# Kernel optimization log

Measured on AMD Instinct MI355X. Metric: run time of the kernel, lower is better.

Reference implementation:

```python
import jax, jax.numpy as jnp
import numpy as np

N = 4096
FIN = 512
HID = 256
NCLS = 2
NE = 131072

def _glorot(key, fan_in, fan_out):
    r = np.sqrt(6.0 / (fan_in + fan_out))
    return jax.random.uniform(key, (fan_in, fan_out), jnp.float32, -r, r)

def setup_inputs() -> dict:
    key = jax.random.key(0)
    ks = jax.random.split(key, 16)
    X = jax.random.normal(ks[0], (N, FIN), jnp.float32)
    adj_rows = jax.random.randint(ks[1], (NE,), 0, N, jnp.int32)
    adj_cols = jax.random.randint(ks[2], (NE,), 0, N, jnp.int32)
    adj_vals = jax.random.uniform(ks[3], (NE,), jnp.float32)
    W_shared = _glorot(ks[4], FIN, HID)
    W_iv = _glorot(ks[5], HID, HID)
    W_c = _glorot(ks[6], HID, HID)
    W_r = _glorot(ks[7], HID, HID)
    Wg_iv = _glorot(ks[8], HID, HID)
    Wg_c = _glorot(ks[9], HID, HID)
    Wg_r = _glorot(ks[10], HID, HID)
    lin_W = _glorot(ks[11], 2 * HID, NCLS)
    lin_b = jnp.zeros((NCLS,), jnp.float32)
    return {"X": X, "adj_rows": adj_rows, "adj_cols": adj_cols, "adj_vals": adj_vals,
            "W_shared": W_shared, "W_iv": W_iv, "W_c": W_c, "W_r": W_r,
            "Wg_iv": Wg_iv, "Wg_c": Wg_c, "Wg_r": Wg_r, "lin_W": lin_W, "lin_b": lin_b}

def _spmm(rows, cols, vals, m):
    # sparse.mm(adj, m): out[i] = sum_{e: rows[e]==i} vals[e] * m[cols[e]]
    return jax.ops.segment_sum(vals[:, None] * m[cols], rows, num_segments=N)

def _gcn(x, rows, cols, vals, W):
    # dropout is identity in eval mode
    return jax.nn.relu(_spmm(rows, cols, vals, x @ W))

def _graphite(x, r1, r2, W):
    h = x @ W
    return jax.nn.relu(r1 @ (r1.T @ h) + r2 @ (r2.T @ h))

def reference(X, adj_rows, adj_cols, adj_vals, W_shared, W_iv, W_c, W_r, Wg_iv, Wg_c, Wg_r, lin_W, lin_b):
    h = _gcn(X, adj_rows, adj_cols, adj_vals, W_shared)
    z_iv0 = _gcn(h, adj_rows, adj_cols, adj_vals, W_iv)
    z_c0 = _gcn(h, adj_rows, adj_cols, adj_vals, W_c)
    z_r0 = _gcn(h, adj_rows, adj_cols, adj_vals, W_r)
    z_iv_rec0 = z_iv0 @ z_iv0.T
    z_c_rec0 = z_c0 @ z_c0.T
    z_r_rec0 = z_r0 @ z_r0.T
    A_dense = jnp.zeros((N, N), jnp.float32).at[adj_rows, adj_cols].add(adj_vals)
    z_iv = _graphite(z_iv0, A_dense, jax.nn.sigmoid(z_iv_rec0), Wg_iv)
    z_c = _graphite(z_c0, A_dense, jax.nn.sigmoid(z_c_rec0), Wg_c)
    z_r = _graphite(z_r0, A_dense, jax.nn.sigmoid(z_r_rec0), Wg_r)
    z_iv_rec = z_iv @ z_iv.T
    z_c_rec = z_c @ z_c.T
    z_r_rec = z_r @ z_r.T
    concat = jnp.concatenate([z_iv, z_c], axis=1)
    pred_T = jax.nn.log_softmax(concat @ lin_W + lin_b, axis=1)
    mi_total_loss = jnp.array(0.0, jnp.float32)
    return (z_iv, z_iv_rec, z_c, z_c_rec, z_r, z_r_rec, mi_total_loss, pred_T)
```

## Files before the change

### kernel.cpp

```cpp
#include <hip/hip_runtime.h>

#define Nn   4096
#define FINd 512
#define HIDd 256
#define NEd  131072

typedef unsigned short u16;
typedef __bf16 bf16x8 __attribute__((ext_vector_type(8)));
typedef float floatx4 __attribute__((ext_vector_type(4)));

__device__ __forceinline__ float bf2f(u16 u) {
  union { unsigned int i; float f; } v; v.i = ((unsigned int)u) << 16; return v.f;
}
__device__ __forceinline__ u16 f2bf(float f) {
  union { unsigned int i; float f; } v; v.f = f;
  unsigned int x = v.i;
  return (u16)((x + 0x7FFFu + ((x >> 16) & 1u)) >> 16);
}

#define GLDS(gp, lp) __builtin_amdgcn_global_load_lds( \
    (__attribute__((address_space(1))) unsigned int*)(void*)(gp), \
    (__attribute__((address_space(3))) unsigned int*)(lp), 16, 0, 0)

__global__ __launch_bounds__(256) void hist_priv_k(const int* __restrict__ rows,
                                                   const int* __restrict__ cols,
                                                   int* __restrict__ slabs) {
  __shared__ int cnt[8192];
  const int t = threadIdx.x;
  for (int i = t; i < 8192; i += 256) cnt[i] = 0;
  __syncthreads();
  int base = blockIdx.x * 4096;
  for (int i = t; i < 4096; i += 256) {
    int e = base + i;
    atomicAdd(&cnt[rows[e]], 1);
    atomicAdd(&cnt[4096 + cols[e]], 1);
  }
  __syncthreads();
  int* out = slabs + blockIdx.x * 8192;
  for (int i = t; i < 8192; i += 256) out[i] = cnt[i];
}

__global__ __launch_bounds__(1024) void scan2_k(const unsigned int* __restrict__ X,
                                                const int* __restrict__ slabs,
                                                int* __restrict__ rp, int* __restrict__ cp,
                                                int* __restrict__ rfill, int* __restrict__ cfill,
                                                int* __restrict__ flag) {
  __shared__ int part[1024];
  __shared__ int dcnt;
  const int t = threadIdx.x;
  if (t == 0) dcnt = 0;
  __syncthreads();
  int local = 0;
  for (int i = t; i < 4096; i += 1024) {
    unsigned e = (X[i] >> 7) & 0xFFu;
    if (e >= 100u && e <= 140u) local++;
  }
  if (local) atomicAdd(&dcnt, local);
  int base = t * 8, s = 0, loc[8];
  int csum[8];
#pragma unroll
  for (int j = 0; j < 8; ++j) csum[j] = 0;
  for (int sl = 0; sl < 32; ++sl) {
    const int* sp = slabs + sl * 8192 + base;
#pragma unroll
    for (int j = 0; j < 8; ++j) csum[j] += sp[j];
  }
#pragma unroll
  for (int j = 0; j < 8; ++j) { loc[j] = s; s += csum[j]; }
  part[t] = s;
  __syncthreads();
  if (t == 0) *flag = (dcnt > 2458) ? 1 : 0;
  for (int off = 1; off < 1024; off <<= 1) {
    int v = (t >= off) ? part[t - off] : 0;
    __syncthreads();
    part[t] += v;
    __syncthreads();
  }
  int excl = (t == 0) ? 0 : part[t - 1];
  int rtot = part[511];
  if (t < 512) {
#pragma unroll
    for (int j = 0; j < 8; ++j) rp[base + j] = excl + loc[j];
    if (t == 511) rp[4096] = rtot;
  } else {
    int cb = base - 4096;
    int ex2 = excl - rtot;
#pragma unroll
    for (int j = 0; j < 8; ++j) cp[cb + j] = ex2 + loc[j];
    if (t == 1023) cp[4096] = part[1023] - rtot;
  }
  for (int i = t; i < 4096; i += 1024) { rfill[i] = 0; cfill[i] = 0; }
}

__global__ __launch_bounds__(256) void setup2_k(const void* __restrict__ X,
                                                const void* __restrict__ Wsh,
                                                const void* __restrict__ W0, const void* __restrict__ W1,
                                                const void* __restrict__ W2, const void* __restrict__ G0,
                                                const void* __restrict__ G1, const void* __restrict__ G2,
                                                const void* __restrict__ linW, const void* __restrict__ linb,
                                                const int* __restrict__ rows, const int* __restrict__ cols,
                                                const void* __restrict__ vals,
                                                const int* __restrict__ rp, const int* __restrict__ cp,
                                                int* __restrict__ rfill, int* __restrict__ cfill,
                                                int2* __restrict__ rpack, int2* __restrict__ cpack,
                                                u16* __restrict__ Xb, u16* __restrict__ WshT,
                                                u16* __restrict__ WTb, u16* __restrict__ WgTb,
                                                float* __restrict__ linWf, float* __restrict__ linbf,
                                                const int* __restrict__ flag) {
  int fl = *flag;
  int bx = blockIdx.x;
  if (bx >= 10245) {
    int e = (bx - 10245) * 256 + threadIdx.x;
    if (e >= NEd) return;
    float v = fl ? bf2f(((const u16*)vals)[e]) : ((const float*)vals)[e];
    int r = rows[e], c = cols[e];
    int p1 = rp[r] + atomicAdd(&rfill[r], 1);
    rpack[p1] = make_int2(c, __float_as_int(v));
    int p2 = cp[c] + atomicAdd(&cfill[c], 1);
    cpack[p2] = make_int2(r, __float_as_int(v));
    return;
  }
  int i = bx * 256 + threadIdx.x;
  if (i < 2097152) {
    Xb[i] = fl ? ((const u16*)X)[i] : f2bf(((const float*)X)[i]);
    return;
  }
  int i2 = i - 2097152;
  if (i2 < 131072) {
    int r = i2 >> 8, c = i2 & 255;
    u16 v = fl ? ((const u16*)Wsh)[i2] : f2bf(((const float*)Wsh)[i2]);
    WshT[c * 512 + r] = v;
    return;
  }
  int i3 = i2 - 131072;
  if (i3 < 393216) {
    int w = i3 >> 16, j = i3 & 65535;
    int r = j >> 8, c = j & 255;
    const void* src = (w == 0) ? W0 : (w == 1) ? W1 : (w == 2) ? W2
                     : (w == 3) ? G0 : (w == 4) ? G1 : G2;
    u16 v = fl ? ((const u16*)src)[j] : f2bf(((const float*)src)[j]);
    u16* dst = (w < 3) ? (WTb + w * 65536) : (WgTb + (w - 3) * 65536);
    dst[c * 256 + r] = v;
    return;
  }
  int i4 = i3 - 393216;
  if (i4 < 1024) { linWf[i4] = fl ? bf2f(((const u16*)linW)[i4]) : ((const float*)linW)[i4]; return; }
  if (i4 < 1026) { int k = i4 - 1024; linbf[k] = fl ? bf2f(((const u16*)linb)[k]) : ((const float*)linb)[k]; }
}

struct SPP {
  const int* ptr; const int2* ep;
  const u16* m[3]; u16* ob[3]; unsigned long long oo[3];
};
__global__ __launch_bounds__(256) void spmm_mb_k(SPP s, const float* __restrict__ part,
                                                 void* __restrict__ outbase, int mode,
                                                 const int* __restrict__ flag) {
  const int b = blockIdx.y;
  int gid = blockIdx.x * 256 + threadIdx.x;
  int row = gid >> 6, lane = gid & 63, f = lane << 2;
  int beg = s.ptr[row], end = s.ptr[row + 1];
  const u16* m = s.m[b];
  float ax = 0.f, ay = 0.f, az = 0.f, aw = 0.f;
  for (int e = beg; e < end; ++e) {
    int2 cv = s.ep[e];
    float v = __int_as_float(cv.y);
    ushort4 mv = *(const ushort4*)(m + (size_t)cv.x * HIDd + f);
    ax = fmaf(v, bf2f(mv.x), ax);
    ay = fmaf(v, bf2f(mv.y), ay);
    az = fmaf(v, bf2f(mv.z), az);
    aw = fmaf(v, bf2f(mv.w), aw);
  }
  size_t o = (size_t)row * HIDd + f;
  if (mode == 2) {
    const float* pb = part + (size_t)b * 1048576 + o;
    float4 p0 = *(const float4*)(pb);
    float4 p1 = *(const float4*)(pb + 3145728);
    float4 p2 = *(const float4*)(pb + 2 * 3145728);
    float4 p3 = *(const float4*)(pb + 3 * 3145728);
    ax += p0.x + p1.x + p2.x + p3.x;
    ay += p0.y + p1.y + p2.y + p3.y;
    az += p0.z + p1.z + p2.z + p3.z;
    aw += p0.w + p1.w + p2.w + p3.w;
    ax = fmaxf(ax, 0.f); ay = fmaxf(ay, 0.f);
    az = fmaxf(az, 0.f); aw = fmaxf(aw, 0.f);
    ushort4 o4 = { f2bf(ax), f2bf(ay), f2bf(az), f2bf(aw) };
    *(ushort4*)(s.ob[b] + o) = o4;
    if (*flag) *(ushort4*)((u16*)outbase + s.oo[b] + o) = o4;
    else       *(float4*)((float*)outbase + s.oo[b] + o) = make_float4(ax, ay, az, aw);
  } else {
    if (mode == 0) {
      ax = fmaxf(ax, 0.f); ay = fmaxf(ay, 0.f);
      az = fmaxf(az, 0.f); aw = fmaxf(aw, 0.f);
    }
    ushort4 o4 = { f2bf(ax), f2bf(ay), f2bf(az), f2bf(aw) };
    *(ushort4*)(s.ob[b] + o) = o4;
  }
}

struct RSU {
  const float* part; u16* tT;
  const int* cp; const int2* cep;
  const u16* hp[3]; u16* ub[3];
};
__global__ __launch_bounds__(256) void redt_spmmu_k(RSU r) {
  int bx = blockIdx.x;
  if (bx < 3072) {
    int i = (bx * 256 + threadIdx.x) * 4;
    float4 s0 = *(const float4*)(r.part + i);
    float4 s1 = *(const float4*)(r.part + i + 3145728);
    float4 s2 = *(const float4*)(r.part + i + 2 * 3145728);
    float4 s3 = *(const float4*)(r.part + i + 3 * 3145728);
    ushort4 o = { f2bf(s0.x + s1.x + s2.x + s3.x), f2bf(s0.y + s1.y + s2.y + s3.y),
                  f2bf(s0.z + s1.z + s2.z + s3.z), f2bf(s0.w + s1.w + s2.w + s3.w) };
    *(ushort4*)(r.tT + i) = o;
    return;
  }
  int bb = (bx - 3072) >> 10;
  int gid = ((bx - 3072) & 1023) * 256 + threadIdx.x;
  int row = gid >> 6, lane = gid & 63, f = lane << 2;
  int beg = r.cp[row], end = r.cp[row + 1];
  const u16* m = r.hp[bb];
  float ax = 0.f, ay = 0.f, az = 0.f, aw = 0.f;
  for (int e = beg; e < end; ++e) {
    int2 cv = r.cep[e];
    float v = __int_as_float(cv.y);
    ushort4 mv = *(const ushort4*)(m + (size_t)cv.x * HIDd + f);
    ax = fmaf(v, bf2f(mv.x), ax);
    ay = fmaf(v, bf2f(mv.y), ay);
    az = fmaf(v, bf2f(mv.z), az);
    aw = fmaf(v, bf2f(mv.w), aw);
  }
  size_t o = (size_t)row * HIDd + f;
  ushort4 o4 = { f2bf(ax), f2bf(ay), f2bf(az), f2bf(aw) };
  *(ushort4*)(r.ub[bb] + o) = o4;
}

struct Job {
  const u16* A; const u16* B;
  const float* F1; const float* F2;
  unsigned long long c0, c1, pstride;
  int M, N, K, mode, xt, ntiles, nks, kspan, sym;
};
struct Jobs { Job j[6]; };

__global__ __launch_bounds__(256) void gemm_mega(Jobs P, void* __restrict__ WSv,
                                                 void* __restrict__ OutO,
                                                 const int* __restrict__ flag) {
  __shared__ __align__(16) u16 smem[17408];
  u16* As = smem;
  u16* Bs = smem + 8192;
  u16* Ts = smem;
  const Job jb = P.j[blockIdx.z];
  const unsigned tile = blockIdx.x;
  if ((int)tile >= jb.ntiles * jb.nks) return;
  if (jb.mode == 6) {
    int i = tile * 256 + threadIdx.x;
    const float* lw = jb.F1;
    float a0 = jb.F2[0], a1 = jb.F2[1];
    for (int f = 0; f < HIDd; ++f) {
      float zv = bf2f(jb.A[(size_t)i * HIDd + f]);
      a0 = fmaf(zv, lw[2 * f + 0], a0);
      a1 = fmaf(zv, lw[2 * f + 1], a1);
    }
    for (int f = 0; f < HIDd; ++f) {
      float zv = bf2f(jb.B[(size_t)i * HIDd + f]);
      a0 = fmaf(zv, lw[2 * (HIDd + f) + 0], a0);
      a1 = fmaf(zv, lw[2 * (HIDd + f) + 1], a1);
    }
    float mx = fmaxf(a0, a1);
    float lse = mx + logf(expf(a0 - mx) + expf(a1 - mx));
    float p0 = a0 - lse, p1 = a1 - lse;
    if (*flag) {
      u16* ob = (u16*)OutO;
      ob[jb.c0 + 2 * i + 0] = f2bf(p0);
      ob[jb.c0 + 2 * i + 1] = f2bf(p1);
      if (i == 0) ob[jb.c1] = 0;
    } else {
      float* ob = (float*)OutO;
      ob[jb.c0 + 2 * i + 0] = p0;
      ob[jb.c0 + 2 * i + 1] = p1;
      if (i == 0) ob[jb.c1] = 0.f;
    }
    return;
  }
  const unsigned ks = tile / (unsigned)jb.ntiles;
  const unsigned t2 = tile - ks * jb.ntiles;
  unsigned ty, tx;
  if (jb.sym) {
    unsigned rem = t2, rowlen = jb.xt; ty = 0;
    while (rem >= rowlen) { rem -= rowlen; --rowlen; ++ty; }
    tx = ty + rem;
  } else {
    ty = t2 / (unsigned)jb.xt;
    tx = t2 - ty * jb.xt;
  }
  const int K = jb.K, N = jb.N;
  const int row0 = ty * 128, col0 = tx * 128;
  const int tid = threadIdx.x;
  const int w = tid >> 6, lane = tid & 63;
  const int wr = (w >> 1) * 64, wc = (w & 1) * 64;
  const int lr = lane >> 3, cc = lane & 7;
  const int scol = (cc ^ lr) << 3;
  floatx4 acc[4][4] = {};
  int aoff[4], boff[4];
#pragma unroll
  for (int i = 0; i < 4; ++i) {
    int m = wr + i * 16 + (lane & 15);
    aoff[i] = m * 64 + ((((lane >> 4) << 3)) ^ ((m & 7) << 3));
    int n = wc + i * 16 + (lane & 15);
    boff[i] = n * 64 + ((((lane >> 4) << 3)) ^ ((n & 7) << 3));
  }
  const u16* A = jb.A;
  const u16* B = jb.B;
  const int kbeg = ks * jb.kspan, kend = kbeg + jb.kspan;
  for (int k0 = kbeg; k0 < kend; k0 += 64) {
#pragma unroll
    for (int t = 0; t < 4; ++t) {
      int ch = 4 * w + t;
      GLDS(A + (size_t)(row0 + 8 * ch + lr) * K + k0 + scol, As + ch * 512);
      GLDS(B + (size_t)(col0 + 8 * ch + lr) * K + k0 + scol, Bs + ch * 512);
    }
    __syncthreads();
#pragma unroll
    for (int kk = 0; kk < 2; ++kk) {
      bf16x8 af[4], bfr[4];
#pragma unroll
      for (int i = 0; i < 4; ++i) {
        af[i]  = *(const bf16x8*)(As + (aoff[i] ^ (kk << 5)));
        bfr[i] = *(const bf16x8*)(Bs + (boff[i] ^ (kk << 5)));
      }
#pragma unroll
      for (int i = 0; i < 4; ++i)
#pragma unroll
        for (int j = 0; j < 4; ++j)
          acc[i][j] = __builtin_amdgcn_mfma_f32_16x16x32_bf16(af[i], bfr[j], acc[i][j], 0, 0, 0);
    }
    __syncthreads();
  }

  const int l15 = lane & 15, q4 = (lane >> 4) << 2;
  const int cb = col0 + wc + l15;
  const int mode = jb.mode;
  if (mode == 5) {
    float* C = (float*)WSv + jb.c0 + (size_t)ks * jb.pstride;
#pragma unroll
    for (int i = 0; i < 4; ++i)
#pragma unroll
      for (int r = 0; r < 4; ++r) {
        size_t rb = (size_t)(row0 + wr + i * 16 + q4 + r) * N + cb;
#pragma unroll
        for (int j = 0; j < 4; ++j) C[rb + j * 16] = acc[i][j][r];
      }
  } else if (mode == 0 || mode == 1) {
    u16* C = ((mode == 1) ? (u16*)OutO : (u16*)WSv) + jb.c0;
#pragma unroll
    for (int i = 0; i < 4; ++i)
#pragma unroll
      for (int r = 0; r < 4; ++r) {
        int lrow = wr + i * 16 + q4 + r;
        size_t rb = (size_t)(row0 + lrow) * N + cb;
#pragma unroll
        for (int j = 0; j < 4; ++j) {
          float v = acc[i][j][r];
          if (mode == 1) v = 1.f / (1.f + __expf(-v));
          u16 vb = f2bf(v);
          C[rb + j * 16] = vb;
          if (jb.sym) Ts[(wc + j * 16 + l15) * 136 + lrow] = vb;
        }
      }
    if (jb.sym && tx != ty) {
      __syncthreads();
      int rr = tid >> 1, hf = (tid & 1) << 6;
      size_t rb2 = (size_t)(col0 + rr) * N + row0 + hf;
#pragma unroll
      for (int k = 0; k < 8; ++k)
        *(uint4*)(C + rb2 + k * 8) = *(const uint4*)(Ts + rr * 136 + hf + k * 8);
    }
  } else if (mode == 4) {
    u16* C  = (u16*)WSv + jb.c0;
    u16* CT = (u16*)WSv + jb.c1;
    const int M = jb.M;
#pragma unroll
    for (int i = 0; i < 4; ++i)
#pragma unroll
      for (int r = 0; r < 4; ++r) {
        int gr = row0 + wr + i * 16 + q4 + r;
#pragma unroll
        for (int j = 0; j < 4; ++j) {
          u16 v = f2bf(acc[i][j][r]);
          int gc = cb + j * 16;
          C[(size_t)gr * N + gc] = v;
          CT[(size_t)gc * M + gr] = v;
        }
      }
  } else {
    if (*flag) {
      u16* C = (u16*)OutO + jb.c0;
#pragma unroll
      for (int i = 0; i < 4; ++i)
#pragma unroll
        for (int r = 0; r < 4; ++r) {
          int lrow = wr + i * 16 + q4 + r;
          size_t rb = (size_t)(row0 + lrow) * N + cb;
#pragma unroll
          for (int j = 0; j < 4; ++j) {
            u16 vb = f2bf(acc[i][j][r]);
            C[rb + j * 16] = vb;
            if (jb.sym) Ts[(wc + j * 16 + l15) * 136 + lrow] = vb;
          }
        }
      if (jb.sym && tx != ty) {
        __syncthreads();
        int rr = tid >> 1, hf = (tid & 1) << 6;
        size_t rb2 = (size_t)(col0 + rr) * N + row0 + hf;
#pragma unroll
        for (int k = 0; k < 8; ++k)
          *(uint4*)(C + rb2 + k * 8) = *(const uint4*)(Ts + rr * 136 + hf + k * 8);
      }
    } else {
      float* C = (float*)OutO + jb.c0;
#pragma unroll
      for (int i = 0; i < 4; ++i)
#pragma unroll
        for (int r = 0; r < 4; ++r) {
          int gr = row0 + wr + i * 16 + q4 + r;
          size_t rb = (size_t)gr * N + cb;
#pragma unroll
          for (int j = 0; j < 4; ++j) C[rb + j * 16] = acc[i][j][r];
        }
      if (jb.sym && tx != ty) {
        float* Tf = (float*)smem;
        const int whalf = w & 1;
#pragma unroll
        for (int half = 0; half < 2; ++half) {
          __syncthreads();
          if (whalf == half) {
#pragma unroll
            for (int i = 0; i < 4; ++i)
#pragma unroll
              for (int j = 0; j < 4; ++j) {
                int cl = j * 16 + l15;
#pragma unroll
                for (int r = 0; r < 4; ++r)
                  Tf[cl * 132 + wr + i * 16 + q4 + r] = acc[i][j][r];
              }
          }
          __syncthreads();
          int cl = tid >> 2, chf = (tid & 3) << 5;
          size_t rb2 = (size_t)(col0 + half * 64 + cl) * N + row0 + chf;
          const float* src = Tf + cl * 132 + chf;
#pragma unroll
          for (int k = 0; k < 8; ++k)
            *(float4*)(C + rb2 + k * 4) = *(const float4*)(src + k * 4);
        }
      }
    }
  }
}

extern "C" void kernel_launch(void* const* d_in, const int* in_sizes, int n_in,
                              void* d_out, int out_size, void* d_ws, size_t ws_size,
                              hipStream_t stream) {
  const void* X    = d_in[0];
  const int*  rows = (const int*)d_in[1];
  const int*  cols = (const int*)d_in[2];
  const void* vals = d_in[3];
  const void* Wsh  = d_in[4];

  char* W = (char*)d_ws;
  u16*  Xb    = (u16*)(W + 0);
  u16*  WshT  = (u16*)(W + 4194304);
  u16*  WTb   = (u16*)(W + 4456448);
  u16*  WgTb  = (u16*)(W + 4849664);
  int*  rp    = (int*)(W + 5242880);
  int*  cp    = (int*)(W + 5275648);
  int*  rfill = (int*)(W + 5308416);
  int*  cfill = (int*)(W + 5324800);
  int2* rpack = (int2*)(W + 5341184);
  int2* cpack = (int2*)(W + 6389760);
  float* linWf = (float*)(W + 7438336);
  float* linbf = (float*)(W + 7442432);
  int*  flag  = (int*)(W + 7442560);
  u16*  hb    = (u16*)(W + 8388608);
  u16*  tmpb[3] = { (u16*)(W + 10485760), (u16*)(W + 12582912), (u16*)(W + 14680064) };
  u16*  z0b[3]  = { (u16*)(W + 16777216), (u16*)(W + 18874368), (u16*)(W + 20971520) };
  u16*  hpb[3]  = { (u16*)(W + 23068672), (u16*)(W + 25165824), (u16*)(W + 27262976) };
  u16*  hpT[3]  = { (u16*)(W + 29360128), (u16*)(W + 31457280), (u16*)(W + 33554432) };
  u16*  tTb     = (u16*)(W + 35651584);
  u16*  zbb[3]  = { (u16*)(W + 41943040), (u16*)(W + 44040192), (u16*)(W + 46137344) };
  u16*  ubb[3]  = { (u16*)(W + 48234496), (u16*)(W + 50331648), (u16*)(W + 52428800) };
  float* partf  = (float*)(W + 54525952);
  int*  slabs  = (int*)(W + 54525952);
  const unsigned long long part_e0 = 54525952ULL / 4;

  const long long z_off[3]   = { 0LL, 17825792LL, 35651584LL };
  const long long rec_off[3] = { 1048576LL, 18874368LL, 36700160LL };
  const long long mi_off = 53477376LL, pred_off = 53477377LL;

  const u16* r2p[3] = { (const u16*)d_out + rec_off[0], (const u16*)d_out + rec_off[1],
                        (const u16*)d_out + rec_off[2] };

  hist_priv_k<<<32, 256, 0, stream>>>(rows, cols, slabs);
  scan2_k<<<1, 1024, 0, stream>>>((const unsigned int*)X, slabs, rp, cp, rfill, cfill, flag);
  setup2_k<<<10757, 256, 0, stream>>>(X, Wsh, d_in[5], d_in[6], d_in[7],
                                      d_in[8], d_in[9], d_in[10], d_in[11], d_in[12],
                                      rows, cols, vals, rp, cp, rfill, cfill, rpack, cpack,
                                      Xb, WshT, WTb, WgTb, linWf, linbf, flag);

  Jobs P{};
  auto setj = [](Job& j, const u16* A, const u16* B, unsigned long long c0,
                 unsigned long long c1, unsigned long long ps, int M, int N, int K,
                 int mode, int nks, int sym) {
    j.A = A; j.B = B; j.F1 = nullptr; j.F2 = nullptr;
    j.c0 = c0; j.c1 = c1; j.pstride = ps;
    j.M = M; j.N = N; j.K = K; j.mode = mode;
    j.xt = N / 128;
    j.ntiles = sym ? (j.xt * (j.xt + 1)) / 2 : (M / 128) * (N / 128);
    j.nks = nks; j.kspan = K / nks; j.sym = sym;
  };

  setj(P.j[0], Xb, WshT, ((char*)tmpb[0] - W) / 2, 0, 0, Nn, HIDd, FINd, 0, 1, 0);
  gemm_mega<<<dim3(64, 1, 1), 256, 0, stream>>>(P, d_ws, d_out, flag);

  SPP s{};
  s.ptr = rp; s.ep = rpack;
  s.m[0] = tmpb[0]; s.ob[0] = hb;
  spmm_mb_k<<<dim3(Nn / 4, 1), 256, 0, stream>>>(s, nullptr, nullptr, 0, flag);

  for (int b = 0; b < 3; ++b)
    setj(P.j[b], hb, WTb + b * 65536, ((char*)tmpb[b] - W) / 2, 0, 0, Nn, HIDd, HIDd, 0, 1, 0);
  gemm_mega<<<dim3(64, 1, 3), 256, 0, stream>>>(P, d_ws, d_out, flag);

  for (int b = 0; b < 3; ++b) { s.m[b] = tmpb[b]; s.ob[b] = z0b[b]; }
  spmm_mb_k<<<dim3(Nn / 4, 3), 256, 0, stream>>>(s, nullptr, nullptr, 0, flag);

  for (int b = 0; b < 3; ++b) {
    setj(P.j[b], z0b[b], z0b[b], rec_off[b], 0, 0, Nn, Nn, HIDd, 1, 1, 1);
    setj(P.j[3 + b], z0b[b], WgTb + b * 65536, ((char*)hpb[b] - W) / 2,
         ((char*)hpT[b] - W) / 2, 0, Nn, HIDd, HIDd, 4, 1, 0);
  }
  gemm_mega<<<dim3(528, 1, 6), 256, 0, stream>>>(P, d_ws, d_out, flag);

  for (int b = 0; b < 3; ++b)
    setj(P.j[b], hpT[b], r2p[b], part_e0 + (unsigned long long)b * 1048576, 0, 3145728,
         HIDd, Nn, Nn, 5, 4, 0);
  gemm_mega<<<dim3(256, 1, 3), 256, 0, stream>>>(P, d_ws, d_out, flag);

  RSU r{};
  r.part = partf; r.tT = tTb; r.cp = cp; r.cep = cpack;
  for (int b = 0; b < 3; ++b) { r.hp[b] = hpb[b]; r.ub[b] = ubb[b]; }
  redt_spmmu_k<<<6144, 256, 0, stream>>>(r);

  for (int b = 0; b < 3; ++b)
    setj(P.j[b], r2p[b], tTb + b * 1048576, part_e0 + (unsigned long long)b * 1048576, 0,
         3145728, Nn, HIDd, Nn, 5, 4, 0);
  gemm_mega<<<dim3(256, 1, 3), 256, 0, stream>>>(P, d_ws, d_out, flag);

  for (int b = 0; b < 3; ++b) {
    s.m[b] = ubb[b];
    s.ob[b] = zbb[b]; s.oo[b] = (unsigned long long)z_off[b];
  }
  spmm_mb_k<<<dim3(Nn / 4, 3), 256, 0, stream>>>(s, partf, d_out, 2, flag);

  for (int b = 0; b < 3; ++b)
    setj(P.j[b], zbb[b], zbb[b], rec_off[b], 0, 0, Nn, Nn, HIDd, 3, 1, 1);
  setj(P.j[3], zbb[0], zbb[1], (unsigned long long)pred_off,
       (unsigned long long)mi_off, 0, 256, 128, 64, 6, 1, 0);
  P.j[3].ntiles = 16; P.j[3].nks = 1;
  P.j[3].F1 = linWf; P.j[3].F2 = linbf;
  gemm_mega<<<dim3(528, 1, 4), 256, 0, stream>>>(P, d_ws, d_out, flag);

  (void)in_sizes; (void)n_in; (void)out_size; (void)ws_size;
}
```

Before: 697.1 us.

## Add dedicated tall-skinny split-K GEMM kernel for graphite projections

Replaces the two split-K mode-5 gemm_mega launches (256xN and Nx256 products against the 4096x4096 sigmoid matrix) with a new 512-thread gemm_tall kernel. Each block covers the full 256-wide side with a 256x128 tile, so the large matrix is streamed once per stripe instead of being reloaded for each 128-wide tile of the thin dimension. The cost is more shared memory per block and fewer, larger blocks, which may lower occupancy. Like the old path it still uses a single-buffered pipeline with no prefetch.

```diff
diff --git a/kernel.cpp b/kernel.cpp
--- a/kernel.cpp
+++ b/kernel.cpp
@@ -235,6 +235,80 @@
   *(ushort4*)(r.ub[bb] + o) = o4;
 }
 
+struct TallP { const u16* Ap[3]; const u16* Bp[3]; unsigned long long c0[3];
+               int tallA, K, N, kspan; };
+
+__global__ __launch_bounds__(512) void gemm_tall(TallP P, float* __restrict__ partf) {
+  __shared__ __align__(16) u16 smem[24576];
+  const int b = blockIdx.z;
+  const u16* A = P.Ap[b];
+  const u16* B = P.Bp[b];
+  const int K = P.K, N = P.N, tallA = P.tallA;
+  const int stripe = blockIdx.x & 31, ks = blockIdx.x >> 5;
+  const int tid = threadIdx.x, w = tid >> 6, lane = tid & 63;
+  const int lr = lane >> 3, cc = lane & 7;
+  const int scol = (cc ^ lr) << 3;
+  u16* As = smem;
+  u16* Bs = smem + (tallA ? 16384 : 8192);
+  int wrow, wcol;
+  if (tallA) { wrow = (w >> 1) * 64; wcol = (w & 1) * 64; }
+  else       { wrow = (w >> 2) * 64; wcol = (w & 3) * 64; }
+  const int row0 = tallA ? 0 : stripe * 128;
+  const int col0 = tallA ? stripe * 128 : 0;
+  const int na = tallA ? 4 : 2;
+  const int nb = tallA ? 2 : 4;
+  floatx4 acc[4][4] = {};
+  int aoff[4], boff[4];
+#pragma unroll
+  for (int i = 0; i < 4; ++i) {
+    int m = wrow + i * 16 + (lane & 15);
+    aoff[i] = m * 64 + (((lane >> 4) << 3) ^ ((m & 7) << 3));
+    int n = wcol + i * 16 + (lane & 15);
+    boff[i] = n * 64 + (((lane >> 4) << 3) ^ ((n & 7) << 3));
+  }
+  const int kbeg = ks * P.kspan, kend = kbeg + P.kspan;
+  for (int k0 = kbeg; k0 < kend; k0 += 64) {
+#pragma unroll
+    for (int t = 0; t < 4; ++t) {
+      if (t < na) {
+        int ch = na * w + t;
+        GLDS(A + (size_t)(row0 + 8 * ch + lr) * K + k0 + scol, As + ch * 512);
+      }
+      if (t < nb) {
+        int ch = nb * w + t;
+        GLDS(B + (size_t)(col0 + 8 * ch + lr) * K + k0 + scol, Bs + ch * 512);
+      }
+    }
+    __syncthreads();
+#pragma unroll
+    for (int kk = 0; kk < 2; ++kk) {
+      bf16x8 af[4], bfr[4];
+#pragma unroll
+      for (int i = 0; i < 4; ++i) {
+        af[i]  = *(const bf16x8*)(As + (aoff[i] ^ (kk << 5)));
+        bfr[i] = *(const bf16x8*)(Bs + (boff[i] ^ (kk << 5)));
+      }
+#pragma unroll
+      for (int i = 0; i < 4; ++i)
+#pragma unroll
+        for (int j = 0; j < 4; ++j)
+          acc[i][j] = __builtin_amdgcn_mfma_f32_16x16x32_bf16(af[i], bfr[j], acc[i][j], 0, 0, 0);
+    }
+    __syncthreads();
+  }
+  const int l15 = lane & 15, q4 = (lane >> 4) << 2;
+  float* C = partf + P.c0[b] + (size_t)ks * 3145728;
+  const int cbase = col0 + wcol + l15;
+#pragma unroll
+  for (int i = 0; i < 4; ++i)
+#pragma unroll
+    for (int r = 0; r < 4; ++r) {
+      size_t rb = (size_t)(row0 + wrow + i * 16 + q4 + r) * N + cbase;
+#pragma unroll
+      for (int j = 0; j < 4; ++j) C[rb + j * 16] = acc[i][j][r];
+    }
+}
+
 struct Job {
   const u16* A; const u16* B;
   const float* F1; const float* F2;
@@ -341,17 +415,7 @@
   const int l15 = lane & 15, q4 = (lane >> 4) << 2;
   const int cb = col0 + wc + l15;
   const int mode = jb.mode;
-  if (mode == 5) {
-    float* C = (float*)WSv + jb.c0 + (size_t)ks * jb.pstride;
-#pragma unroll
-    for (int i = 0; i < 4; ++i)
-#pragma unroll
-      for (int r = 0; r < 4; ++r) {
-        size_t rb = (size_t)(row0 + wr + i * 16 + q4 + r) * N + cb;
-#pragma unroll
-        for (int j = 0; j < 4; ++j) C[rb + j * 16] = acc[i][j][r];
-      }
-  } else if (mode == 0 || mode == 1) {
+  if (mode == 0 || mode == 1) {
     u16* C = ((mode == 1) ? (u16*)OutO : (u16*)WSv) + jb.c0;
 #pragma unroll
     for (int i = 0; i < 4; ++i)
@@ -491,7 +555,6 @@
   u16*  ubb[3]  = { (u16*)(W + 48234496), (u16*)(W + 50331648), (u16*)(W + 52428800) };
   float* partf  = (float*)(W + 54525952);
   int*  slabs  = (int*)(W + 54525952);
-  const unsigned long long part_e0 = 54525952ULL / 4;
 
   const long long z_off[3]   = { 0LL, 17825792LL, 35651584LL };
   const long long rec_off[3] = { 1048576LL, 18874368LL, 36700160LL };
@@ -541,20 +604,26 @@
   }
   gemm_mega<<<dim3(528, 1, 6), 256, 0, stream>>>(P, d_ws, d_out, flag);
 
-  for (int b = 0; b < 3; ++b)
-    setj(P.j[b], hpT[b], r2p[b], part_e0 + (unsigned long long)b * 1048576, 0, 3145728,
-         HIDd, Nn, Nn, 5, 4, 0);
-  gemm_mega<<<dim3(256, 1, 3), 256, 0, stream>>>(P, d_ws, d_out, flag);
+  TallP T{};
+  for (int b = 0; b < 3; ++b) {
+    T.Ap[b] = hpT[b]; T.Bp[b] = r2p[b];
+    T.c0[b] = (unsigned long long)b * 1048576ULL;
+  }
+  T.tallA = 1; T.K = Nn; T.N = Nn; T.kspan = 1024;
+  gemm_tall<<<dim3(128, 1, 3), 512, 0, stream>>>(T, partf);
 
   RSU r{};
   r.part = partf; r.tT = tTb; r.cp = cp; r.cep = cpack;
   for (int b = 0; b < 3; ++b) { r.hp[b] = hpb[b]; r.ub[b] = ubb[b]; }
   redt_spmmu_k<<<6144, 256, 0, stream>>>(r);
 
-  for (int b = 0; b < 3; ++b)
-    setj(P.j[b], r2p[b], tTb + b * 1048576, part_e0 + (unsigned long long)b * 1048576, 0,
-         3145728, Nn, HIDd, Nn, 5, 4, 0);
-  gemm_mega<<<dim3(256, 1, 3), 256, 0, stream>>>(P, d_ws, d_out, flag);
+  TallP T2{};
+  for (int b = 0; b < 3; ++b) {
+    T2.Ap[b] = r2p[b]; T2.Bp[b] = tTb + b * 1048576;
+    T2.c0[b] = (unsigned long long)b * 1048576ULL;
+  }
+  T2.tallA = 0; T2.K = Nn; T2.N = HIDd; T2.kspan = 1024;
+  gemm_tall<<<dim3(128, 1, 3), 512, 0, stream>>>(T2, partf);
 
   for (int b = 0; b < 3; ++b) {
     s.m[b] = ubb[b];
```

After: 681.6 us. 1.02x faster.
